# Kernel tuning notes

Measured on AMD Instinct MI355X. Metric: run time of the kernel, lower is better.

Reference implementation:

```python
import jax, jax.numpy as jnp
import numpy as np

NQ = 8    # QCNN qubits
NLQ = 4   # QLSTM qubits == hidden_dim
C64 = jnp.complex64

H_GATE = (1.0 / np.sqrt(2.0)) * jnp.array([[1, 1], [1, -1]], dtype=C64)


def ap1(st, U, q):
    # apply 2x2 gate U on qubit axis q of state st (shape (2,)*n)
    s = jnp.moveaxis(st, q, -1)
    s = jnp.einsum('ij,...j->...i', U, s)
    return jnp.moveaxis(s, -1, q)


def apcx(st, c, t):
    # CNOT with control c, target t: flip target slice where control == 1
    s = jnp.moveaxis(st, (c, t), (-2, -1))
    s = jnp.stack([s[..., 0, :], s[..., 1, ::-1]], axis=-2)
    return jnp.moveaxis(s, (-2, -1), (c, t))


def RX(t):
    c = jnp.cos(t / 2).astype(C64)
    s = (-1j * jnp.sin(t / 2)).astype(C64)
    return jnp.stack([jnp.stack([c, s]), jnp.stack([s, c])])


def RY(t):
    c = jnp.cos(t / 2)
    s = jnp.sin(t / 2)
    return jnp.stack([jnp.stack([c, -s]), jnp.stack([s, c])]).astype(C64)


def RZ(t):
    e = jnp.exp(-0.5j * t).astype(C64)
    z = jnp.zeros((), C64)
    return jnp.stack([jnp.stack([e, z]), jnp.stack([z, jnp.conj(e)])])


def PH(t):
    # qiskit phase gate P(t) = diag(1, e^{i t})
    e = jnp.exp(1j * t).astype(C64)
    o = jnp.ones((), C64)
    z = jnp.zeros((), C64)
    return jnp.stack([jnp.stack([o, z]), jnp.stack([z, e])])


def init_state(n):
    st = jnp.zeros((2,) * n, C64)
    return st.at[(0,) * n].set(1.0)


def zexp(st, q):
    # <Z_q> of statevector st
    p = st.real ** 2 + st.imag ** 2
    m = p.sum(axis=tuple(a for a in range(st.ndim) if a != q))
    return m[0] - m[1]


def conv_block(st, p, q1, q2):
    st = ap1(st, RZ(-np.pi / 2), q2)
    st = apcx(st, q2, q1)
    st = ap1(st, RZ(p[0]), q1)
    st = ap1(st, RY(p[1]), q2)
    st = apcx(st, q1, q2)
    st = ap1(st, RY(p[2]), q2)
    st = apcx(st, q2, q1)
    st = ap1(st, RZ(np.pi / 2), q1)
    return st


def pool_block(st, p, src, sink):
    st = ap1(st, RZ(-np.pi / 2), sink)
    st = apcx(st, sink, src)
    st = ap1(st, RZ(p[0]), src)
    st = ap1(st, RY(p[1]), sink)
    st = apcx(st, src, sink)
    st = ap1(st, RY(p[2]), sink)
    return st


QCNN_SPECS = [
    (conv_block, [(0, 1), (2, 3), (4, 5), (6, 7)]),  # c1
    (pool_block, [(0, 1), (2, 3), (4, 5), (6, 7)]),  # p1
    (conv_block, [(0, 1), (2, 3)]),                  # c2
    (pool_block, [(0, 1), (2, 3)]),                  # p2
    (conv_block, [(0, 1)]),                          # c3
    (pool_block, [(0, 1)]),                          # p3
]


def qcnn_single(x, w):
    # x: (8,) feature angles, w: (42,) ansatz weights
    st = init_state(NQ)
    for _ in range(2):
        for q in range(NQ):
            st = ap1(st, H_GATE, q)
        for q in range(NQ):
            st = ap1(st, PH(2.0 * x[q]), q)
    idx = 0
    for blk, prs in QCNN_SPECS:
        for a, b in prs:
            st = blk(st, w[idx:idx + 3], a, b)
            idx += 3
    return zexp(st, NQ - 1)  # 'ZIIIIIII' => Z on qubit 7 (little-endian)


def qgate_single(v, theta):
    # v: (4,) encoder angles (per sample), theta: (4,) trainable RX angles
    st = init_state(NLQ)
    for i in range(NLQ):
        st = ap1(st, RX(v[i]), i)
    for i in range(NLQ):
        st = ap1(st, RX(theta[i]), i)
    for i in range(NLQ - 1):
        st = apcx(st, i, i + 1)
    st = apcx(st, NLQ - 1, 0)
    return jnp.stack([zexp(st, q) for q in range(NLQ)])


qgate = jax.vmap(qgate_single, in_axes=(0, None))


def setup_inputs() -> dict:
    key = jax.random.key(0)
    ks = jax.random.split(key, 12)
    B, S = 16, 128
    x = jax.random.uniform(ks[0], (B, S, NQ), jnp.float32) * np.pi
    qcnn_w = jax.random.normal(ks[1], (42,), jnp.float32) * 0.1

    def lin(k, out_d, in_d):
        k1, k2 = jax.random.split(k)
        lim = 1.0 / np.sqrt(in_d)
        W = jax.random.uniform(k1, (out_d, in_d), jnp.float32, -lim, lim)
        b = jax.random.uniform(k2, (out_d,), jnp.float32, -lim, lim)
        return W, b

    Wf, bf = lin(ks[2], NLQ, 1 + NLQ)
    Wi, bi = lin(ks[3], NLQ, 1 + NLQ)
    Wg, bg = lin(ks[4], NLQ, 1 + NLQ)
    Wo, bo = lin(ks[5], NLQ, 1 + NLQ)
    theta_f = jax.random.normal(ks[6], (NLQ,), jnp.float32) * 0.1
    theta_i = jax.random.normal(ks[7], (NLQ,), jnp.float32) * 0.1
    theta_g = jax.random.normal(ks[8], (NLQ,), jnp.float32) * 0.1
    theta_o = jax.random.normal(ks[9], (NLQ,), jnp.float32) * 0.1
    Wh, bh = lin(ks[10], 1, NLQ)
    return dict(x=x, qcnn_w=qcnn_w, theta_f=theta_f, theta_i=theta_i,
                theta_g=theta_g, theta_o=theta_o, Wf=Wf, bf=bf, Wi=Wi, bi=bi,
                Wg=Wg, bg=bg, Wo=Wo, bo=bo, Wh=Wh, bh=bh)


def reference(x, qcnn_w, theta_f, theta_i, theta_g, theta_o,
              Wf, bf, Wi, bi, Wg, bg, Wo, bo, Wh, bh):
    B, S, _ = x.shape
    flat = x.reshape(B * S, NQ)
    qcnn_out = jax.vmap(qcnn_single, in_axes=(0, None))(flat, qcnn_w)
    qcnn_out = qcnn_out.reshape(B, S, 1)
    lstm_in = jnp.transpose(qcnn_out, (1, 0, 2))  # (S, B, 1)
    h0 = jnp.zeros((B, NLQ), x.dtype)
    c0 = jnp.zeros((B, NLQ), x.dtype)

    def step(carry, xt):
        hx, cx = carry
        comb = jnp.concatenate([xt, hx], axis=1)  # (B, 1 + hidden)
        f = jax.nn.sigmoid(qgate(comb @ Wf.T + bf, theta_f))
        i = jax.nn.sigmoid(qgate(comb @ Wi.T + bi, theta_i))
        g = jnp.tanh(qgate(comb @ Wg.T + bg, theta_g))
        o = jax.nn.sigmoid(qgate(comb @ Wo.T + bo, theta_o))
        cx = f * cx + i * g
        hx = o * jnp.tanh(cx)
        return (hx, cx), hx

    _, outs = jax.lax.scan(step, (h0, c0), lstm_in)  # outs: (S, B, hidden)
    logits = outs[-1] @ Wh.T + bh  # (B, 1)
    return qcnn_out, logits
```

## Files before the change

kernel.cpp:

```cpp
#include <hip/hip_runtime.h>
#include <math.h>

#define PI_F 3.14159265358979323846f

__device__ __forceinline__ float rcpf(float x) { return __builtin_amdgcn_rcpf(x); }
__device__ __forceinline__ void fswap(float2& p, float2& q) { float2 t = p; p = q; q = t; }


template<int Q>
__device__ __forceinline__ float exq(float v) {
    if constexpr (Q == 2)
        return __int_as_float(__builtin_amdgcn_update_dpp(0, __float_as_int(v), 0xB1, 0xF, 0xF, true));
    else if constexpr (Q == 3)
        return __int_as_float(__builtin_amdgcn_update_dpp(0, __float_as_int(v), 0x4E, 0xF, 0xF, true));
    else if constexpr (Q == 4)
        return __int_as_float(__builtin_amdgcn_ds_swizzle(__float_as_int(v), 0x101F));
    else if constexpr (Q == 5)
        return __int_as_float(__builtin_amdgcn_ds_swizzle(__float_as_int(v), 0x201F));
    else if constexpr (Q == 6)
        return __int_as_float(__builtin_amdgcn_ds_swizzle(__float_as_int(v), 0x401F));
    else
        return __shfl_xor(v, 32, 64);
}

template<int Q>
__device__ __forceinline__ void rzg(float2 a[4], float th, int lane) {
    float c = __cosf(0.5f * th), s = __sinf(0.5f * th);
    if constexpr (Q >= 2) {
        float se = ((lane >> (Q - 2)) & 1) ? s : -s;
        #pragma unroll
        for (int r = 0; r < 4; ++r) {
            float nx = c * a[r].x - se * a[r].y;
            float ny = c * a[r].y + se * a[r].x;
            a[r] = make_float2(nx, ny);
        }
    } else {
        #pragma unroll
        for (int r = 0; r < 4; ++r) {
            int bit = (Q == 0) ? (r >> 1) : (r & 1);
            float se = bit ? s : -s;
            float nx = c * a[r].x - se * a[r].y;
            float ny = c * a[r].y + se * a[r].x;
            a[r] = make_float2(nx, ny);
        }
    }
}

template<int Q>
__device__ __forceinline__ void ryg(float2 a[4], float th, int lane) {
    float c = __cosf(0.5f * th), s = __sinf(0.5f * th);
    if constexpr (Q >= 2) {
        float se = ((lane >> (Q - 2)) & 1) ? s : -s;
        #pragma unroll
        for (int r = 0; r < 4; ++r) {
            float ox = exq<Q>(a[r].x), oy = exq<Q>(a[r].y);
            a[r] = make_float2(c * a[r].x + se * ox, c * a[r].y + se * oy);
        }
    } else if constexpr (Q == 0) {
        #pragma unroll
        for (int r = 0; r < 2; ++r) {
            float2 lo = a[r], hi = a[r + 2];
            a[r]     = make_float2(c * lo.x - s * hi.x, c * lo.y - s * hi.y);
            a[r + 2] = make_float2(s * lo.x + c * hi.x, s * lo.y + c * hi.y);
        }
    } else {
        #pragma unroll
        for (int r = 0; r < 4; r += 2) {
            float2 lo = a[r], hi = a[r + 1];
            a[r]     = make_float2(c * lo.x - s * hi.x, c * lo.y - s * hi.y);
            a[r + 1] = make_float2(s * lo.x + c * hi.x, s * lo.y + c * hi.y);
        }
    }
}

template<int C, int T>
__device__ __forceinline__ void cxg(float2 a[4], int lane) {
    if constexpr (C >= 2) {
        bool cb = (lane >> (C - 2)) & 1;
        #pragma unroll
        for (int r = 0; r < 4; ++r) {
            float ox = exq<T>(a[r].x), oy = exq<T>(a[r].y);
            a[r].x = cb ? ox : a[r].x;
            a[r].y = cb ? oy : a[r].y;
        }
    } else if constexpr (C == 0 && T == 1) {
        fswap(a[2], a[3]);
    } else {
        fswap(a[1], a[3]);
    }
}

template<int Q>
__device__ __forceinline__ void featg(float2 a[4], float xq, int lane) {
    float phi = 2.0f * xq;
    float e1x = __cosf(phi), e1y = __sinf(phi);
    float e2x = e1x * e1x - e1y * e1y;
    float e2y = 2.0f * e1x * e1y;
    float2 u00 = make_float2(0.5f * (1.0f + e1x),  0.5f * e1y);
    float2 u01 = make_float2(0.5f * (1.0f - e1x), -0.5f * e1y);
    float2 u10 = make_float2(0.5f * (e1x - e2x), 0.5f * (e1y - e2y));
    float2 u11 = make_float2(0.5f * (e1x + e2x), 0.5f * (e1y + e2y));
    if constexpr (Q >= 2) {
        bool bset = (lane >> (Q - 2)) & 1;
        float csx = bset ? u11.x : u00.x, csy = bset ? u11.y : u00.y;
        float cox = bset ? u10.x : u01.x, coy = bset ? u10.y : u01.y;
        #pragma unroll
        for (int r = 0; r < 4; ++r) {
            float ox = exq<Q>(a[r].x), oy = exq<Q>(a[r].y);
            float nx = csx * a[r].x - csy * a[r].y + cox * ox - coy * oy;
            float ny = csx * a[r].y + csy * a[r].x + cox * oy + coy * ox;
            a[r] = make_float2(nx, ny);
        }
    } else {
        float2 l, h;
        #define APPL(LO, HI)                                                        \
            l = a[LO]; h = a[HI];                                                   \
            a[LO] = make_float2(u00.x*l.x - u00.y*l.y + u01.x*h.x - u01.y*h.y,      \
                                u00.x*l.y + u00.y*l.x + u01.x*h.y + u01.y*h.x);     \
            a[HI] = make_float2(u10.x*l.x - u10.y*l.y + u11.x*h.x - u11.y*h.y,      \
                                u10.x*l.y + u10.y*l.x + u11.x*h.y + u11.y*h.x);
        if constexpr (Q == 0) { APPL(0, 2) APPL(1, 3) }
        else                  { APPL(0, 1) APPL(2, 3) }
        #undef APPL
    }
}

template<int Q1, int Q2>
__device__ __forceinline__ void convg(float2 a[4], const float* __restrict__ p, int lane) {
    rzg<Q2>(a, -0.5f * PI_F, lane);
    cxg<Q2, Q1>(a, lane);
    rzg<Q1>(a, p[0], lane);
    ryg<Q2>(a, p[1], lane);
    cxg<Q1, Q2>(a, lane);
    ryg<Q2>(a, p[2], lane);
    cxg<Q2, Q1>(a, lane);
    rzg<Q1>(a, 0.5f * PI_F, lane);
}

template<int Q1, int Q2>
__device__ __forceinline__ void poolg(float2 a[4], const float* __restrict__ p, int lane) {
    rzg<Q2>(a, -0.5f * PI_F, lane);
    cxg<Q2, Q1>(a, lane);
    rzg<Q1>(a, p[0], lane);
    ryg<Q2>(a, p[1], lane);
    cxg<Q1, Q2>(a, lane);
    ryg<Q2>(a, p[2], lane);
}

__global__ __launch_bounds__(256) void qcnn_kernel(const float* __restrict__ x,
                                                   const float* __restrict__ w,
                                                   float* __restrict__ out) {
    int lane = threadIdx.x & 63;
    int n = blockIdx.x * 4 + (threadIdx.x >> 6);
    float2 a[4];
    a[0] = make_float2(lane == 0 ? 1.0f : 0.0f, 0.0f);
    a[1] = make_float2(0.0f, 0.0f);
    a[2] = make_float2(0.0f, 0.0f);
    a[3] = make_float2(0.0f, 0.0f);

    const float* xr = x + n * 8;
    featg<0>(a, xr[0], lane);
    featg<1>(a, xr[1], lane);
    featg<2>(a, xr[2], lane);
    featg<3>(a, xr[3], lane);
    featg<4>(a, xr[4], lane);
    featg<5>(a, xr[5], lane);
    featg<6>(a, xr[6], lane);
    featg<7>(a, xr[7], lane);

    convg<0,1>(a, w + 0,  lane);
    convg<2,3>(a, w + 3,  lane);
    convg<4,5>(a, w + 6,  lane);
    convg<6,7>(a, w + 9,  lane);
    poolg<0,1>(a, w + 12, lane);
    poolg<2,3>(a, w + 15, lane);
    poolg<4,5>(a, w + 18, lane);
    poolg<6,7>(a, w + 21, lane);
    convg<0,1>(a, w + 24, lane);
    convg<2,3>(a, w + 27, lane);
    poolg<0,1>(a, w + 30, lane);
    poolg<2,3>(a, w + 33, lane);
    convg<0,1>(a, w + 36, lane);
    poolg<0,1>(a, w + 39, lane);

    float ssum = 0.f;
    #pragma unroll
    for (int r = 0; r < 4; ++r)
        ssum += a[r].x * a[r].x + a[r].y * a[r].y;
    ssum = (lane & 32) ? -ssum : ssum;
    #pragma unroll
    for (int m = 1; m < 64; m <<= 1)
        ssum += __shfl_xor(ssum, m, 64);
    if (lane == 0) out[n] = ssum;
}


template<int CTRL>
__device__ __forceinline__ float bq(float v) {
    return __int_as_float(__builtin_amdgcn_update_dpp(0, __float_as_int(v), CTRL, 0xF, 0xF, true));
}

__device__ __forceinline__ float pick4(bool b0, bool b1, float a0, float a1, float a2, float a3) {
    float t01 = b0 ? a1 : a0;
    float t23 = b0 ? a3 : a2;
    return b1 ? t23 : t01;
}

__global__ __launch_bounds__(64) void qlstm_kernel(
    const float* __restrict__ qc,
    const float* __restrict__ thf, const float* __restrict__ thi,
    const float* __restrict__ thg, const float* __restrict__ tho,
    const float* __restrict__ Wf, const float* __restrict__ bf,
    const float* __restrict__ Wi, const float* __restrict__ bi,
    const float* __restrict__ Wg, const float* __restrict__ bg,
    const float* __restrict__ Wo, const float* __restrict__ bo,
    const float* __restrict__ Wh, const float* __restrict__ bh,
    float* __restrict__ out) {
    __shared__ __align__(16) float qsh[16 * 132];
    int lane = threadIdx.x;

    const float4* qc4 = (const float4*)qc;
    #pragma unroll
    for (int k = 0; k < 8; ++k) {
        int i = k * 64 + lane;
        float4 v = qc4[i];
        int b = i >> 5;
        int t = (i & 31) << 2;
        *(float4*)&qsh[b * 132 + t] = v;
    }
    __builtin_amdgcn_wave_barrier();

    int b = lane >> 2, q = lane & 3;
    bool qb0 = q & 1, qb1 = q & 2;
    const float* Wp = (q == 0) ? Wf : (q == 1) ? Wi : (q == 2) ? Wg : Wo;
    const float* bp = (q == 0) ? bf : (q == 1) ? bi : (q == 2) ? bg : bo;
    const float* tp = (q == 0) ? thf : (q == 1) ? thi : (q == 2) ? thg : tho;

    float W[20], av[4];
    #pragma unroll
    for (int k = 0; k < 20; ++k) W[k] = Wp[k];
    #pragma unroll
    for (int r = 0; r < 4; ++r) av[r] = bp[r] + tp[r];

    float nA = (q == 2) ? 1.0f : 0.0f;
    float nB = (q == 2) ? -2.0f : 1.0f;
    float nK = (q == 2) ? 2.0f : -1.0f;

    float c = 0.f;
    float h0 = 0.f, h1 = 0.f, h2 = 0.f, h3 = 0.f;
    const float* qrow = &qsh[b * 132];
    float xv = qrow[0];

    for (int t = 0; t < 128; ++t) {
        float xn = qrow[t + 1];
        float vA = av[0] + W[0]*xv  + W[1]*h0  + W[2]*h1  + W[3]*h2  + W[4]*h3;
        float vB = av[1] + W[5]*xv  + W[6]*h0  + W[7]*h1  + W[8]*h2  + W[9]*h3;
        float vC = av[2] + W[10]*xv + W[11]*h0 + W[12]*h1 + W[13]*h2 + W[14]*h3;
        float vD = av[3] + W[15]*xv + W[16]*h0 + W[17]*h1 + W[18]*h2 + W[19]*h3;
        float cA = __cosf(vA), cB = __cosf(vB), cC = __cosf(vC), cD = __cosf(vD);
        float r1 = cA * cB, r2 = r1 * cC, r3 = r2 * cD, r0 = cB * (cC * cD);
        float E0 = __expf(nK * r0), E1 = __expf(nK * r1);
        float E2 = __expf(nK * r2), E3 = __expf(nK * r3);
        float n0 = nA + nB * rcpf(E0 + 1.0f);
        float n1 = nA + nB * rcpf(E1 + 1.0f);
        float n2 = nA + nB * rcpf(E2 + 1.0f);
        float n3 = nA + nB * rcpf(E3 + 1.0f);
        float F0 = bq<0x00>(n0), F1 = bq<0x00>(n1), F2 = bq<0x00>(n2), F3 = bq<0x00>(n3);
        float I0 = bq<0x55>(n0), I1 = bq<0x55>(n1), I2 = bq<0x55>(n2), I3 = bq<0x55>(n3);
        float G0 = bq<0xAA>(n0), G1 = bq<0xAA>(n1), G2 = bq<0xAA>(n2), G3 = bq<0xAA>(n3);
        float O0 = bq<0xFF>(n0), O1 = bq<0xFF>(n1), O2 = bq<0xFF>(n2), O3 = bq<0xFF>(n3);
        float F = pick4(qb0, qb1, F0, F1, F2, F3);
        float I = pick4(qb0, qb1, I0, I1, I2, I3);
        float G = pick4(qb0, qb1, G0, G1, G2, G3);
        float O = pick4(qb0, qb1, O0, O1, O2, O3);
        c = F * c + I * G;
        float Ec = __expf(2.0f * c);
        float tau = 1.0f - 2.0f * rcpf(Ec + 1.0f);
        float hq = O * tau;
        h0 = bq<0x00>(hq);
        h1 = bq<0x55>(hq);
        h2 = bq<0xAA>(hq);
        h3 = bq<0xFF>(hq);
        xv = xn;
    }

    if (q == 0)
        out[2048 + b] = bh[0] + Wh[0]*h0 + Wh[1]*h1 + Wh[2]*h2 + Wh[3]*h3;
}

extern "C" void kernel_launch(void* const* d_in, const int* in_sizes, int n_in,
                              void* d_out, int out_size, void* d_ws, size_t ws_size,
                              hipStream_t stream) {
    const float* x = (const float*)d_in[0];
    const float* w = (const float*)d_in[1];
    float* out = (float*)d_out;

    qcnn_kernel<<<512, 256, 0, stream>>>(x, w, out);
    qlstm_kernel<<<1, 64, 0, stream>>>(
        out,
        (const float*)d_in[2], (const float*)d_in[3],
        (const float*)d_in[4], (const float*)d_in[5],
        (const float*)d_in[6], (const float*)d_in[7],
        (const float*)d_in[8], (const float*)d_in[9],
        (const float*)d_in[10], (const float*)d_in[11],
        (const float*)d_in[12], (const float*)d_in[13],
        (const float*)d_in[14], (const float*)d_in[15],
        out);
}
```

Before: 121.9 us.

## Fuse QCNN and QLSTM into one launch with epoch-keyed spin-wait flags

Merges the two kernels into a single 513-block launch. The last block waits on per-sample 64-bit flags in workspace, each packing a QCNN result with an epoch-derived key, then runs the LSTM recurrence and bumps the epoch counter. The change removes the second launch and the gap between kernels, and replaces the shfl_xor reduction with DPP, swizzle and permlane32_swap. It relies on the consumer block making forward progress alongside the producers, and on the workspace epoch staying consistent across calls. A stale flag value that happens to match the key could let it read wrong data.

```diff
diff --git a/kernel.cpp b/kernel.cpp
--- a/kernel.cpp
+++ b/kernel.cpp
@@ -2,6 +2,9 @@
 #include <math.h>
 
 #define PI_F 3.14159265358979323846f
+#define FLAG_MAGIC 0x9E3779B9u
+
+typedef int v2i __attribute__((ext_vector_type(2)));
 
 __device__ __forceinline__ float rcpf(float x) { return __builtin_amdgcn_rcpf(x); }
 __device__ __forceinline__ void fswap(float2& p, float2& q) { float2 t = p; p = q; q = t; }
@@ -19,8 +22,10 @@
         return __int_as_float(__builtin_amdgcn_ds_swizzle(__float_as_int(v), 0x201F));
     else if constexpr (Q == 6)
         return __int_as_float(__builtin_amdgcn_ds_swizzle(__float_as_int(v), 0x401F));
-    else
-        return __shfl_xor(v, 32, 64);
+    else {
+        v2i r = __builtin_amdgcn_permlane32_swap(__float_as_int(v), __float_as_int(v), false, false);
+        return __int_as_float((threadIdx.x & 32) ? r[0] : r[1]);
+    }
 }
 
 template<int Q>
@@ -147,54 +152,6 @@
     ryg<Q2>(a, p[2], lane);
 }
 
-__global__ __launch_bounds__(256) void qcnn_kernel(const float* __restrict__ x,
-                                                   const float* __restrict__ w,
-                                                   float* __restrict__ out) {
-    int lane = threadIdx.x & 63;
-    int n = blockIdx.x * 4 + (threadIdx.x >> 6);
-    float2 a[4];
-    a[0] = make_float2(lane == 0 ? 1.0f : 0.0f, 0.0f);
-    a[1] = make_float2(0.0f, 0.0f);
-    a[2] = make_float2(0.0f, 0.0f);
-    a[3] = make_float2(0.0f, 0.0f);
-
-    const float* xr = x + n * 8;
-    featg<0>(a, xr[0], lane);
-    featg<1>(a, xr[1], lane);
-    featg<2>(a, xr[2], lane);
-    featg<3>(a, xr[3], lane);
-    featg<4>(a, xr[4], lane);
-    featg<5>(a, xr[5], lane);
-    featg<6>(a, xr[6], lane);
-    featg<7>(a, xr[7], lane);
-
-    convg<0,1>(a, w + 0,  lane);
-    convg<2,3>(a, w + 3,  lane);
-    convg<4,5>(a, w + 6,  lane);
-    convg<6,7>(a, w + 9,  lane);
-    poolg<0,1>(a, w + 12, lane);
-    poolg<2,3>(a, w + 15, lane);
-    poolg<4,5>(a, w + 18, lane);
-    poolg<6,7>(a, w + 21, lane);
-    convg<0,1>(a, w + 24, lane);
-    convg<2,3>(a, w + 27, lane);
-    poolg<0,1>(a, w + 30, lane);
-    poolg<2,3>(a, w + 33, lane);
-    convg<0,1>(a, w + 36, lane);
-    poolg<0,1>(a, w + 39, lane);
-
-    float ssum = 0.f;
-    #pragma unroll
-    for (int r = 0; r < 4; ++r)
-        ssum += a[r].x * a[r].x + a[r].y * a[r].y;
-    ssum = (lane & 32) ? -ssum : ssum;
-    #pragma unroll
-    for (int m = 1; m < 64; m <<= 1)
-        ssum += __shfl_xor(ssum, m, 64);
-    if (lane == 0) out[n] = ssum;
-}
-
-
 template<int CTRL>
 __device__ __forceinline__ float bq(float v) {
     return __int_as_float(__builtin_amdgcn_update_dpp(0, __float_as_int(v), CTRL, 0xF, 0xF, true));
@@ -206,8 +163,9 @@
     return b1 ? t23 : t01;
 }
 
-__global__ __launch_bounds__(64) void qlstm_kernel(
-    const float* __restrict__ qc,
+
+__global__ __launch_bounds__(256) void fused_kernel(
+    const float* __restrict__ x,  const float* __restrict__ w,
     const float* __restrict__ thf, const float* __restrict__ thi,
     const float* __restrict__ thg, const float* __restrict__ tho,
     const float* __restrict__ Wf, const float* __restrict__ bf,
@@ -215,18 +173,80 @@
     const float* __restrict__ Wg, const float* __restrict__ bg,
     const float* __restrict__ Wo, const float* __restrict__ bo,
     const float* __restrict__ Wh, const float* __restrict__ bh,
-    float* __restrict__ out) {
+    float* __restrict__ out, unsigned long long* __restrict__ flg) {
     __shared__ __align__(16) float qsh[16 * 132];
-    int lane = threadIdx.x;
-
-    const float4* qc4 = (const float4*)qc;
-    #pragma unroll
-    for (int k = 0; k < 8; ++k) {
-        int i = k * 64 + lane;
-        float4 v = qc4[i];
-        int b = i >> 5;
-        int t = (i & 31) << 2;
-        *(float4*)&qsh[b * 132 + t] = v;
+    int lane = threadIdx.x & 63;
+    int wave = threadIdx.x >> 6;
+    unsigned* epoch = (unsigned*)(flg + 2048);
+
+    if (blockIdx.x != 512) {
+        unsigned key = FLAG_MAGIC ^ __hip_atomic_load(epoch, __ATOMIC_RELAXED, __HIP_MEMORY_SCOPE_AGENT);
+        int n = blockIdx.x * 4 + wave;
+        float2 a[4];
+        a[0] = make_float2(lane == 0 ? 1.0f : 0.0f, 0.0f);
+        a[1] = make_float2(0.0f, 0.0f);
+        a[2] = make_float2(0.0f, 0.0f);
+        a[3] = make_float2(0.0f, 0.0f);
+
+        const float* xr = x + n * 8;
+        featg<0>(a, xr[0], lane);
+        featg<1>(a, xr[1], lane);
+        featg<2>(a, xr[2], lane);
+        featg<3>(a, xr[3], lane);
+        featg<4>(a, xr[4], lane);
+        featg<5>(a, xr[5], lane);
+        featg<6>(a, xr[6], lane);
+        featg<7>(a, xr[7], lane);
+
+        convg<0,1>(a, w + 0,  lane);
+        convg<2,3>(a, w + 3,  lane);
+        convg<4,5>(a, w + 6,  lane);
+        convg<6,7>(a, w + 9,  lane);
+        poolg<0,1>(a, w + 12, lane);
+        poolg<2,3>(a, w + 15, lane);
+        poolg<4,5>(a, w + 18, lane);
+        poolg<6,7>(a, w + 21, lane);
+        convg<0,1>(a, w + 24, lane);
+        convg<2,3>(a, w + 27, lane);
+        poolg<0,1>(a, w + 30, lane);
+        poolg<2,3>(a, w + 33, lane);
+        convg<0,1>(a, w + 36, lane);
+        poolg<0,1>(a, w + 39, lane);
+
+        float ssum = 0.f;
+        #pragma unroll
+        for (int r = 0; r < 4; ++r)
+            ssum += a[r].x * a[r].x + a[r].y * a[r].y;
+        ssum = (lane & 32) ? -ssum : ssum;
+        ssum += exq<2>(ssum);
+        ssum += exq<3>(ssum);
+        ssum += exq<4>(ssum);
+        ssum += exq<5>(ssum);
+        ssum += exq<6>(ssum);
+        {
+            v2i rr = __builtin_amdgcn_permlane32_swap(__float_as_int(ssum), __float_as_int(ssum), false, false);
+            ssum = __int_as_float((threadIdx.x & 32) ? rr[0] : rr[1]) +
+                   __int_as_float((threadIdx.x & 32) ? rr[1] : rr[0]);
+        }
+        if (lane == 0) {
+            out[n] = ssum;
+            unsigned long long pk = ((unsigned long long)__float_as_uint(ssum) << 32)
+                                  | (unsigned long long)key;
+            __hip_atomic_store(&flg[n], pk, __ATOMIC_RELAXED, __HIP_MEMORY_SCOPE_AGENT);
+        }
+        return;
+    }
+
+    if (wave != 0) return;
+    unsigned key = FLAG_MAGIC ^ __hip_atomic_load(epoch, __ATOMIC_RELAXED, __HIP_MEMORY_SCOPE_AGENT);
+
+    for (int j = 0; j < 32; ++j) {
+        int idx = j * 64 + lane;
+        unsigned long long v;
+        do {
+            v = __hip_atomic_load(&flg[idx], __ATOMIC_RELAXED, __HIP_MEMORY_SCOPE_AGENT);
+        } while ((unsigned)v != key);
+        qsh[(idx >> 7) * 132 + (idx & 127)] = __uint_as_float((unsigned)(v >> 32));
     }
     __builtin_amdgcn_wave_barrier();
 
@@ -286,24 +306,22 @@
 
     if (q == 0)
         out[2048 + b] = bh[0] + Wh[0]*h0 + Wh[1]*h1 + Wh[2]*h2 + Wh[3]*h3;
+
+    if (lane == 0)
+        __hip_atomic_fetch_add(epoch, 1u, __ATOMIC_RELAXED, __HIP_MEMORY_SCOPE_AGENT);
 }
 
 extern "C" void kernel_launch(void* const* d_in, const int* in_sizes, int n_in,
                               void* d_out, int out_size, void* d_ws, size_t ws_size,
                               hipStream_t stream) {
-    const float* x = (const float*)d_in[0];
-    const float* w = (const float*)d_in[1];
-    float* out = (float*)d_out;
-
-    qcnn_kernel<<<512, 256, 0, stream>>>(x, w, out);
-    qlstm_kernel<<<1, 64, 0, stream>>>(
-        out,
-        (const float*)d_in[2], (const float*)d_in[3],
-        (const float*)d_in[4], (const float*)d_in[5],
-        (const float*)d_in[6], (const float*)d_in[7],
-        (const float*)d_in[8], (const float*)d_in[9],
+    fused_kernel<<<513, 256, 0, stream>>>(
+        (const float*)d_in[0],  (const float*)d_in[1],
+        (const float*)d_in[2],  (const float*)d_in[3],
+        (const float*)d_in[4],  (const float*)d_in[5],
+        (const float*)d_in[6],  (const float*)d_in[7],
+        (const float*)d_in[8],  (const float*)d_in[9],
         (const float*)d_in[10], (const float*)d_in[11],
         (const float*)d_in[12], (const float*)d_in[13],
         (const float*)d_in[14], (const float*)d_in[15],
-        out);
-}
+        (float*)d_out, (unsigned long long*)d_ws);
+}
```

New measurement: 129.3 us. 1.06x slower.
